# Kernel tuning notes

Hardware: AMD Instinct MI355X
Metric: run time of the kernel (lower is better)

The kernel has to match this reference:

```python
import jax, jax.numpy as jnp
import numpy as np

EPS = 1e-7  # keras backend epsilon


def setup_inputs() -> dict:
    key = jax.random.key(0)
    k1, k2, k3, k4, k5 = jax.random.split(key, 5)
    B, L, D, U = 8, 1024, 256, 256
    seq_data = jax.random.normal(k1, (B, L, D), dtype=jnp.float32)
    graph = jax.random.uniform(k2, (B, L, L), dtype=jnp.float32)
    scale = 1.0 / np.sqrt(D)
    e_weight = jax.random.normal(k3, (D, U), dtype=jnp.float32) * scale
    Wx = jax.random.normal(k4, (U, U), dtype=jnp.float32) * scale
    Wh = jax.random.normal(k5, (U, U), dtype=jnp.float32) * scale
    b = jnp.zeros((U,), dtype=jnp.float32)
    return {"seq_data": seq_data, "graph": graph, "e_weight": e_weight,
            "Wx": Wx, "Wh": Wh, "b": b}


def reference(seq_data, graph, e_weight, Wx, Wh, b):
    # beta = seq_data @ e_weight : (B, L, U)
    beta = jnp.einsum('bld,du->blu', seq_data, e_weight)
    # normalize_graph_output: divide by out-degree sum over axis 2 -> (B, L)
    norm = jnp.maximum(jnp.sum(graph, axis=2), EPS)
    beta = beta / norm[:, :, None]
    # K.batch_dot(beta(B,L,U), graph(B,L,M), axes=(1,1)) -> (B,U,M), then
    # permute (0,2,1) -> (B,M,U); fused as a single einsum.
    agg = jnp.einsum('blu,blm->bmu', beta, graph)  # (B, L, U)
    B, L, U = agg.shape
    h0 = jnp.zeros((B, U), dtype=agg.dtype)  # get_initial_state: zeros

    def step(h, x):  # SimpleRNNCell: h' = tanh(x Wx + h Wh + b)
        h = jnp.tanh(x @ Wx + h @ Wh + b)
        return h, h

    _, ys = jax.lax.scan(step, h0, jnp.swapaxes(agg, 0, 1))  # (L, B, U)
    return jnp.swapaxes(ys, 0, 1)  # (B, L, U)
```

## Files before the change

### kernel.cpp

```cpp
#include <hip/hip_runtime.h>
#include <hip/hip_bf16.h>


typedef unsigned short u16;
typedef unsigned int u32;
typedef __bf16 bf16_t;
typedef __bf16 bf16x8 __attribute__((ext_vector_type(8)));
typedef float f32x4 __attribute__((ext_vector_type(4)));
typedef unsigned short u16x8 __attribute__((ext_vector_type(8)));
typedef unsigned short u16x4 __attribute__((ext_vector_type(4)));

#define LDS_P 72
#define HP_B  288

struct HiLo { u16 hi, lo; };

__device__ __forceinline__ u16 f2bf(float f) {
  bf16_t h = (bf16_t)f;
  return __builtin_bit_cast(u16, h);
}
__device__ __forceinline__ HiLo splitf(float v) {
  bf16_t h = (bf16_t)v;
  HiLo r;
  r.hi = __builtin_bit_cast(u16, h);
  r.lo = f2bf(v - (float)h);
  return r;
}
__device__ __forceinline__ float tanh_fast(float x) {
  float ax = fabsf(x);
  float e  = __expf(-2.0f * ax);
  float t  = __fdividef(1.0f - e, 1.0f + e);
  return copysignf(t, x);
}
__device__ __forceinline__ void sync_lds_only() {
  __asm__ volatile("s_waitcnt lgkmcnt(0)\ns_barrier" ::: "memory");
}

__global__ __launch_bounds__(512, 2) void front1(
    const float* __restrict__ Wx, u16* __restrict__ Wxth, u16* __restrict__ Wxtl,
    const float* __restrict__ Wh, u16* __restrict__ Whth, u16* __restrict__ Whtl,
    const float* __restrict__ graph, float* __restrict__ rnorm,
    const float* __restrict__ seq, const float* __restrict__ E,
    u16* __restrict__ betaTh, u16* __restrict__ betaTl) {
  __shared__ u16 Ah[64 * LDS_P], Al[64 * LDS_P];
  __shared__ u16 Bh[128 * LDS_P], Bl[128 * LDS_P];
  const int bid = blockIdx.x;
  const int t = threadIdx.x;

  if (bid >= 256 && bid < 512) {
    const int wbid = bid - 256;
    const int u = ((wbid & 127) << 1) + (t >> 8), d = t & 255;
    const float* s; u16 *dh, *dl;
    if (wbid < 128) { s = Wx; dh = Wxth; dl = Wxtl; }
    else            { s = Wh; dh = Whth; dl = Whtl; }
    HiLo r = splitf(s[d * 256 + u]);
    dh[u * 256 + d] = r.hi;
    dl[u * 256 + d] = r.lo;
    return;
  }
  if (bid >= 512) {
    const int wave = t >> 6, lane = t & 63;
    const int row = (bid - 512) * 8 + wave;
    const float* p = graph + (size_t)row * 1024 + lane * 16;
    float s = 0.f;
#pragma unroll
    for (int c = 0; c < 4; c++) {
      f32x4 v = *(const f32x4*)(p + c * 4);
#pragma unroll
      for (int j = 0; j < 4; j++) s += v[j];
    }
#pragma unroll
    for (int off = 32; off > 0; off >>= 1) s += __shfl_xor(s, off);
    if (lane == 0) rnorm[row] = 1.0f / fmaxf(s, 1e-7f);
    return;
  }

  const int v = bid;
  const int w = t >> 6, lane = t & 63, quad = lane >> 4, l16 = lane & 15;
  const int msub = w & 3, nsub = w >> 2;
  const int r0 = (v >> 1) * 64, n_base = (v & 1) * 128;
  f32x4 acc[4];
#pragma unroll
  for (int i = 0; i < 4; i++) acc[i] = (f32x4){0.f, 0.f, 0.f, 0.f};

  for (int kb = 0; kb < 256; kb += 64) {
#pragma unroll
    for (int cc = 0; cc < 2; cc++) {
      int c = t + cc * 512;
      int r = c >> 4, c4 = c & 15;
      f32x4 vv = *(const f32x4*)(seq + (size_t)(r0 + r) * 256 + kb + c4 * 4);
      u16x4 hi, lo;
#pragma unroll
      for (int j = 0; j < 4; j++) {
        HiLo s = splitf(vv[j]);
        hi[j] = s.hi; lo[j] = s.lo;
      }
      *(u16x4*)(Ah + r * LDS_P + c4 * 4) = hi;
      *(u16x4*)(Al + r * LDS_P + c4 * 4) = lo;
    }
#pragma unroll
    for (int cc = 0; cc < 4; cc++) {
      int c = t + cc * 512;
      int r = c >> 5, c5 = c & 31;
      f32x4 vv = *(const f32x4*)(E + (size_t)(kb + r) * 256 + n_base + c5 * 4);
#pragma unroll
      for (int j = 0; j < 4; j++) {
        HiLo s = splitf(vv[j]);
        Bh[(c5 * 4 + j) * LDS_P + r] = s.hi;
        Bl[(c5 * 4 + j) * LDS_P + r] = s.lo;
      }
    }
    __syncthreads();
#pragma unroll
    for (int kk = 0; kk < 64; kk += 32) {
      bf16x8 ah = __builtin_bit_cast(bf16x8, *(const u16x8*)(Ah + (msub * 16 + l16) * LDS_P + kk + quad * 8));
      bf16x8 al = __builtin_bit_cast(bf16x8, *(const u16x8*)(Al + (msub * 16 + l16) * LDS_P + kk + quad * 8));
#pragma unroll
      for (int tN = 0; tN < 4; tN++) {
        int brow = nsub * 64 + tN * 16 + l16;
        bf16x8 bh = __builtin_bit_cast(bf16x8, *(const u16x8*)(Bh + brow * LDS_P + kk + quad * 8));
        bf16x8 bl = __builtin_bit_cast(bf16x8, *(const u16x8*)(Bl + brow * LDS_P + kk + quad * 8));
        acc[tN] = __builtin_amdgcn_mfma_f32_16x16x32_bf16(ah, bh, acc[tN], 0, 0, 0);
        acc[tN] = __builtin_amdgcn_mfma_f32_16x16x32_bf16(ah, bl, acc[tN], 0, 0, 0);
        acc[tN] = __builtin_amdgcn_mfma_f32_16x16x32_bf16(al, bh, acc[tN], 0, 0, 0);
      }
    }
    __syncthreads();
  }
  const int rbase = r0 + msub * 16 + quad * 4;
  const int bI = rbase >> 10, lI = rbase & 1023;
#pragma unroll
  for (int tN = 0; tN < 4; tN++) {
    int u = n_base + nsub * 64 + tN * 16 + l16;
    u16x4 hv, lv;
#pragma unroll
    for (int i = 0; i < 4; i++) {
      HiLo s = splitf(acc[tN][i]);
      hv[i] = s.hi; lv[i] = s.lo;
    }
    size_t off = ((size_t)bI << 18) + (size_t)u * 1024 + lI;
    *(u16x4*)(betaTh + off) = hv;
    *(u16x4*)(betaTl + off) = lv;
  }
}

__global__ __launch_bounds__(512, 2) void gemm_agg(const float* __restrict__ graph,
                                                   const u16* __restrict__ betaTh,
                                                   const u16* __restrict__ betaTl,
                                                   const float* __restrict__ rnorm,
                                                   float* __restrict__ agg) {
  __shared__ u16 Ah[64 * LDS_P], Al[64 * LDS_P];
  __shared__ u16 Bh[128 * LDS_P], Bl[128 * LDS_P];
  const int t = threadIdx.x;
  const int w = t >> 6, lane = t & 63, quad = lane >> 4, l16 = lane & 15;
  const int msub = w & 3, nsub = w >> 2;
  const int m0 = blockIdx.x * 64, n_base = blockIdx.y * 128, b = blockIdx.z;
  const float* g = graph + (size_t)b * (1024 * 1024);
  const float* rnb = rnorm + b * 1024;
  const size_t bt = (size_t)b << 18;
  f32x4 acc[4];
#pragma unroll
  for (int i = 0; i < 4; i++) acc[i] = (f32x4){0.f, 0.f, 0.f, 0.f};

  for (int kb = 0; kb < 1024; kb += 64) {
#pragma unroll
    for (int cc = 0; cc < 2; cc++) {
      int c = t + cc * 512;
      int r = c >> 4, c4 = c & 15;
      f32x4 vv = *(const f32x4*)(g + (size_t)(kb + r) * 1024 + m0 + c4 * 4);
      float rn = rnb[kb + r];
#pragma unroll
      for (int j = 0; j < 4; j++) {
        HiLo s = splitf(vv[j] * rn);
        Ah[(c4 * 4 + j) * LDS_P + r] = s.hi;
        Al[(c4 * 4 + j) * LDS_P + r] = s.lo;
      }
    }
#pragma unroll
    for (int cc = 0; cc < 2; cc++) {
      int c = t + cc * 512;
      int r = c >> 3, c8 = c & 7;
      *(u16x8*)(Bh + r * LDS_P + c8 * 8) =
          *(const u16x8*)(betaTh + bt + (size_t)(n_base + r) * 1024 + kb + c8 * 8);
      *(u16x8*)(Bl + r * LDS_P + c8 * 8) =
          *(const u16x8*)(betaTl + bt + (size_t)(n_base + r) * 1024 + kb + c8 * 8);
    }
    __syncthreads();
#pragma unroll
    for (int kk = 0; kk < 64; kk += 32) {
      bf16x8 ah = __builtin_bit_cast(bf16x8, *(const u16x8*)(Ah + (msub * 16 + l16) * LDS_P + kk + quad * 8));
      bf16x8 al = __builtin_bit_cast(bf16x8, *(const u16x8*)(Al + (msub * 16 + l16) * LDS_P + kk + quad * 8));
#pragma unroll
      for (int tN = 0; tN < 4; tN++) {
        int brow = nsub * 64 + tN * 16 + l16;
        bf16x8 bh = __builtin_bit_cast(bf16x8, *(const u16x8*)(Bh + brow * LDS_P + kk + quad * 8));
        bf16x8 bl = __builtin_bit_cast(bf16x8, *(const u16x8*)(Bl + brow * LDS_P + kk + quad * 8));
        acc[tN] = __builtin_amdgcn_mfma_f32_16x16x32_bf16(ah, bh, acc[tN], 0, 0, 0);
        acc[tN] = __builtin_amdgcn_mfma_f32_16x16x32_bf16(ah, bl, acc[tN], 0, 0, 0);
        acc[tN] = __builtin_amdgcn_mfma_f32_16x16x32_bf16(al, bh, acc[tN], 0, 0, 0);
      }
    }
    __syncthreads();
  }
  const int mbase = m0 + msub * 16 + quad * 4;
#pragma unroll
  for (int tN = 0; tN < 4; tN++) {
    int u = n_base + nsub * 64 + tN * 16 + l16;
#pragma unroll
    for (int i = 0; i < 4; i++)
      agg[((size_t)b * 1024 + mbase + i) * 256 + u] = acc[tN][i];
  }
}

__global__ __launch_bounds__(512, 2) void gemm_xpre(const float* __restrict__ agg,
                                                    const u16* __restrict__ Wxth,
                                                    const u16* __restrict__ Wxtl,
                                                    const float* __restrict__ bias,
                                                    float* __restrict__ Xpre) {
  __shared__ u16 Ah[64 * LDS_P], Al[64 * LDS_P];
  __shared__ u16 Bh[128 * LDS_P], Bl[128 * LDS_P];
  const int t = threadIdx.x;
  const int w = t >> 6, lane = t & 63, quad = lane >> 4, l16 = lane & 15;
  const int msub = w & 3, nsub = w >> 2;
  const int r0 = blockIdx.x * 64, n_base = blockIdx.y * 128;
  f32x4 acc[4];
#pragma unroll
  for (int i = 0; i < 4; i++) acc[i] = (f32x4){0.f, 0.f, 0.f, 0.f};

  for (int kb = 0; kb < 256; kb += 64) {
#pragma unroll
    for (int cc = 0; cc < 2; cc++) {
      int c = t + cc * 512;
      int r = c >> 4, c4 = c & 15;
      f32x4 vv = *(const f32x4*)(agg + (size_t)(r0 + r) * 256 + kb + c4 * 4);
      u16x4 hi, lo;
#pragma unroll
      for (int j = 0; j < 4; j++) {
        HiLo s = splitf(vv[j]);
        hi[j] = s.hi; lo[j] = s.lo;
      }
      *(u16x4*)(Ah + r * LDS_P + c4 * 4) = hi;
      *(u16x4*)(Al + r * LDS_P + c4 * 4) = lo;
    }
#pragma unroll
    for (int cc = 0; cc < 2; cc++) {
      int c = t + cc * 512;
      int r = c >> 3, c8 = c & 7;
      *(u16x8*)(Bh + r * LDS_P + c8 * 8) =
          *(const u16x8*)(Wxth + (size_t)(n_base + r) * 256 + kb + c8 * 8);
      *(u16x8*)(Bl + r * LDS_P + c8 * 8) =
          *(const u16x8*)(Wxtl + (size_t)(n_base + r) * 256 + kb + c8 * 8);
    }
    __syncthreads();
#pragma unroll
    for (int kk = 0; kk < 64; kk += 32) {
      bf16x8 ah = __builtin_bit_cast(bf16x8, *(const u16x8*)(Ah + (msub * 16 + l16) * LDS_P + kk + quad * 8));
      bf16x8 al = __builtin_bit_cast(bf16x8, *(const u16x8*)(Al + (msub * 16 + l16) * LDS_P + kk + quad * 8));
#pragma unroll
      for (int tN = 0; tN < 4; tN++) {
        int brow = nsub * 64 + tN * 16 + l16;
        bf16x8 bh = __builtin_bit_cast(bf16x8, *(const u16x8*)(Bh + brow * LDS_P + kk + quad * 8));
        bf16x8 bl = __builtin_bit_cast(bf16x8, *(const u16x8*)(Bl + brow * LDS_P + kk + quad * 8));
        acc[tN] = __builtin_amdgcn_mfma_f32_16x16x32_bf16(ah, bh, acc[tN], 0, 0, 0);
        acc[tN] = __builtin_amdgcn_mfma_f32_16x16x32_bf16(ah, bl, acc[tN], 0, 0, 0);
        acc[tN] = __builtin_amdgcn_mfma_f32_16x16x32_bf16(al, bh, acc[tN], 0, 0, 0);
      }
    }
    __syncthreads();
  }
  const int rbase = r0 + msub * 16 + quad * 4;
  const int bI = rbase >> 10;
#pragma unroll
  for (int tN = 0; tN < 4; tN++) {
    int u = n_base + nsub * 64 + tN * 16 + l16;
    float bu = bias[u];
#pragma unroll
    for (int i = 0; i < 4; i++) {
      int mI = (rbase + i) & 1023;
      Xpre[((size_t)mI * 8 + bI) * 256 + u] = acc[tN][i] + bu;
    }
  }
}

__global__ __launch_bounds__(512, 2) void rnn_scan(const u16* __restrict__ Whth,
                                                   const u16* __restrict__ Whtl,
                                                   const float* __restrict__ Xpre,
                                                   float* __restrict__ out) {
  __shared__ u16 h2[2][2 * HP_B];
  const int b = blockIdx.x;
  const int t = threadIdx.x;
  const int w = t >> 6, lane = t & 63, quad = lane >> 4, l16 = lane & 15;
  const int colbase = w * 32;
  const bool epi = (quad < 2);
  const int col_e = colbase + quad * 16 + l16;

  bf16x8 bwh[2][8], bwl[2][8];
#pragma unroll
  for (int tN = 0; tN < 2; tN++) {
    const u16* wph = Whth + (size_t)(colbase + tN * 16 + l16) * 256 + quad * 8;
    const u16* wpl = Whtl + (size_t)(colbase + tN * 16 + l16) * 256 + quad * 8;
#pragma unroll
    for (int kb = 0; kb < 8; kb++) {
      bwh[tN][kb] = __builtin_bit_cast(bf16x8, *(const u16x8*)(wph + kb * 32));
      bwl[tN][kb] = __builtin_bit_cast(bf16x8, *(const u16x8*)(wpl + kb * 32));
    }
  }
  for (int i = t; i < 2 * 2 * HP_B; i += 512) ((u16*)h2)[i] = 0;

  float cb[4];
  if (epi) {
#pragma unroll
    for (int k = 0; k < 4; k++) cb[k] = Xpre[(size_t)k * 2048 + b * 256 + col_e];
  }
  const float* ldp = Xpre + 4 * 2048 + b * 256 + col_e;
  float* outp = out + (size_t)b * 262144 + col_e;
  const u16* rb0 = &h2[0][(l16 & 1) * HP_B + quad * 8];
  const u16* rb1 = &h2[1][(l16 & 1) * HP_B + quad * 8];
  u16* wb0 = &h2[0][0];
  u16* wb1 = &h2[1][0];
  __syncthreads();

  for (int m4 = 0; m4 < 1024; m4 += 4) {
#pragma unroll
    for (int k = 0; k < 4; k++) {
      const int p = k & 1;
      const u16* rb = p ? rb1 : rb0;
      u16* hw = p ? wb0 : wb1;

      bf16x8 af[8];
#pragma unroll
      for (int kb = 0; kb < 8; kb++)
        af[kb] = __builtin_bit_cast(bf16x8, *(const u16x8*)(rb + kb * 32));

      f32x4 a0a = {0.f,0.f,0.f,0.f}, a0b = {0.f,0.f,0.f,0.f};
      f32x4 a1a = {0.f,0.f,0.f,0.f}, a1b = {0.f,0.f,0.f,0.f};
#pragma unroll
      for (int kb = 0; kb < 4; kb++) {
        a0a = __builtin_amdgcn_mfma_f32_16x16x32_bf16(af[kb], bwh[0][kb], a0a, 0, 0, 0);
        a1a = __builtin_amdgcn_mfma_f32_16x16x32_bf16(af[kb], bwh[1][kb], a1a, 0, 0, 0);
        a0b = __builtin_amdgcn_mfma_f32_16x16x32_bf16(af[kb + 4], bwh[0][kb + 4], a0b, 0, 0, 0);
        a1b = __builtin_amdgcn_mfma_f32_16x16x32_bf16(af[kb + 4], bwh[1][kb + 4], a1b, 0, 0, 0);
        a0a = __builtin_amdgcn_mfma_f32_16x16x32_bf16(af[kb], bwl[0][kb], a0a, 0, 0, 0);
        a1a = __builtin_amdgcn_mfma_f32_16x16x32_bf16(af[kb], bwl[1][kb], a1a, 0, 0, 0);
        a0b = __builtin_amdgcn_mfma_f32_16x16x32_bf16(af[kb + 4], bwl[0][kb + 4], a0b, 0, 0, 0);
        a1b = __builtin_amdgcn_mfma_f32_16x16x32_bf16(af[kb + 4], bwl[1][kb + 4], a1b, 0, 0, 0);
      }

      if (epi) {
        float sA0 = quad ? a1a[0] : a0a[0];
        float sA1 = quad ? a1a[1] : a0a[1];
        float sB0 = quad ? a1b[0] : a0b[0];
        float sB1 = quad ? a1b[1] : a0b[1];
        float hi_part = sA0 + sB0;
        float lo_part = sA1 + sB1;
        float x = (hi_part + lo_part) + cb[k];
        float y = tanh_fast(x);
        HiLo s = splitf(y);
        hw[col_e] = s.hi;
        hw[HP_B + col_e] = s.lo;
        *outp = y;
        if (m4 <= 1019 - k) {
          cb[k] = *ldp;
          ldp += 2048;
        }
      }
      outp += 256;
      sync_lds_only();
    }
  }
}

extern "C" void kernel_launch(void* const* d_in, const int* in_sizes, int n_in,
                              void* d_out, int out_size, void* d_ws, size_t ws_size,
                              hipStream_t stream) {
  (void)in_sizes; (void)n_in; (void)out_size; (void)ws_size;
  const float* seq   = (const float*)d_in[0];
  const float* graph = (const float*)d_in[1];
  const float* E     = (const float*)d_in[2];
  const float* Wx    = (const float*)d_in[3];
  const float* Wh    = (const float*)d_in[4];
  const float* bias  = (const float*)d_in[5];
  float* out = (float*)d_out;

  char* w = (char*)d_ws;
  float* rnorm  = (float*)(w + 0);
  u16*   Wxth   = (u16*)(w + 294912);
  u16*   Wxtl   = (u16*)(w + 425984);
  u16*   Whth   = (u16*)(w + 557056);
  u16*   Whtl   = (u16*)(w + 688128);
  u16*   betaTh = (u16*)(w + 819200);
  u16*   betaTl = (u16*)(w + 5013504);
  float* agg    = (float*)(w + 9207808);
  float* Xpre   = (float*)(w + 17596416);

  front1<<<1536, 512, 0, stream>>>(Wx, Wxth, Wxtl, Wh, Whth, Whtl,
                                   graph, rnorm, seq, E, betaTh, betaTl);
  gemm_agg<<<dim3(16, 2, 8), 512, 0, stream>>>(graph, betaTh, betaTl, rnorm, agg);
  gemm_xpre<<<dim3(128, 2), 512, 0, stream>>>(agg, Wxth, Wxtl, bias, Xpre);
  rnn_scan<<<dim3(8), 512, 0, stream>>>(Whth, Whtl, Xpre, out);
}
```

Measured before the change: 773.5 us.

## Fuse agg, Xpre GEMMs and RNN scan into one kernel with per-tile flags

Merges the aggregation GEMM, the input-projection GEMM and the recurrent scan into a single 136-block launch. 128 producer blocks each compute one 64-row m-tile for one batch across both N halves, write Xpre, then bump an atomic counter for that tile. 8 scan blocks spin on the counters, so the serial scan can begin as soon as the first time tiles are ready instead of waiting for both GEMMs to finish. This removes two launch boundaries and overlaps the GEMM work with the latency-bound scan. In exchange each producer block now does twice the work serially, and the design relies on all 136 blocks being co-resident to avoid deadlock.

```diff
diff --git a/kernel.cpp b/kernel.cpp
--- a/kernel.cpp
+++ b/kernel.cpp
@@ -35,19 +35,28 @@
 __device__ __forceinline__ void sync_lds_only() {
   __asm__ volatile("s_waitcnt lgkmcnt(0)\ns_barrier" ::: "memory");
 }
+__device__ __forceinline__ void wait_tile(volatile unsigned int* xpref, int tl) {
+  while (__hip_atomic_load(&xpref[tl], __ATOMIC_ACQUIRE,
+                           __HIP_MEMORY_SCOPE_AGENT) < 8u) {
+    __builtin_amdgcn_s_sleep(4);
+  }
+  __threadfence();
+}
 
 __global__ __launch_bounds__(512, 2) void front1(
     const float* __restrict__ Wx, u16* __restrict__ Wxth, u16* __restrict__ Wxtl,
     const float* __restrict__ Wh, u16* __restrict__ Whth, u16* __restrict__ Whtl,
     const float* __restrict__ graph, float* __restrict__ rnorm,
     const float* __restrict__ seq, const float* __restrict__ E,
-    u16* __restrict__ betaTh, u16* __restrict__ betaTl) {
+    u16* __restrict__ betaTh, u16* __restrict__ betaTl,
+    unsigned int* __restrict__ xpref) {
   __shared__ u16 Ah[64 * LDS_P], Al[64 * LDS_P];
   __shared__ u16 Bh[128 * LDS_P], Bl[128 * LDS_P];
   const int bid = blockIdx.x;
   const int t = threadIdx.x;
 
   if (bid >= 256 && bid < 512) {
+    if (bid == 256 && t < 16) xpref[t] = 0;
     const int wbid = bid - 256;
     const int u = ((wbid & 127) << 1) + (t >> 8), d = t & 255;
     const float* s; u16 *dh, *dl;
@@ -144,151 +153,159 @@
   }
 }
 
-__global__ __launch_bounds__(512, 2) void gemm_agg(const float* __restrict__ graph,
-                                                   const u16* __restrict__ betaTh,
-                                                   const u16* __restrict__ betaTl,
-                                                   const float* __restrict__ rnorm,
-                                                   float* __restrict__ agg) {
+__global__ __launch_bounds__(512, 2) void back_fused(
+    const float* __restrict__ graph,
+    const u16* __restrict__ betaTh, const u16* __restrict__ betaTl,
+    const float* __restrict__ rnorm, float* __restrict__ agg,
+    const u16* __restrict__ Wxth, const u16* __restrict__ Wxtl,
+    const float* __restrict__ bias, float* __restrict__ Xpre,
+    const u16* __restrict__ Whth, const u16* __restrict__ Whtl,
+    float* __restrict__ out, unsigned int* __restrict__ xpref) {
   __shared__ u16 Ah[64 * LDS_P], Al[64 * LDS_P];
   __shared__ u16 Bh[128 * LDS_P], Bl[128 * LDS_P];
+  __shared__ u16 h2[2][2 * HP_B];
+  const int pid = blockIdx.x;
   const int t = threadIdx.x;
-  const int w = t >> 6, lane = t & 63, quad = lane >> 4, l16 = lane & 15;
-  const int msub = w & 3, nsub = w >> 2;
-  const int m0 = blockIdx.x * 64, n_base = blockIdx.y * 128, b = blockIdx.z;
-  const float* g = graph + (size_t)b * (1024 * 1024);
-  const float* rnb = rnorm + b * 1024;
-  const size_t bt = (size_t)b << 18;
-  f32x4 acc[4];
-#pragma unroll
-  for (int i = 0; i < 4; i++) acc[i] = (f32x4){0.f, 0.f, 0.f, 0.f};
-
-  for (int kb = 0; kb < 1024; kb += 64) {
-#pragma unroll
-    for (int cc = 0; cc < 2; cc++) {
-      int c = t + cc * 512;
-      int r = c >> 4, c4 = c & 15;
-      f32x4 vv = *(const f32x4*)(g + (size_t)(kb + r) * 1024 + m0 + c4 * 4);
-      float rn = rnb[kb + r];
-#pragma unroll
-      for (int j = 0; j < 4; j++) {
-        HiLo s = splitf(vv[j] * rn);
-        Ah[(c4 * 4 + j) * LDS_P + r] = s.hi;
-        Al[(c4 * 4 + j) * LDS_P + r] = s.lo;
-      }
-    }
-#pragma unroll
-    for (int cc = 0; cc < 2; cc++) {
-      int c = t + cc * 512;
-      int r = c >> 3, c8 = c & 7;
-      *(u16x8*)(Bh + r * LDS_P + c8 * 8) =
-          *(const u16x8*)(betaTh + bt + (size_t)(n_base + r) * 1024 + kb + c8 * 8);
-      *(u16x8*)(Bl + r * LDS_P + c8 * 8) =
-          *(const u16x8*)(betaTl + bt + (size_t)(n_base + r) * 1024 + kb + c8 * 8);
-    }
+
+  if (pid < 128) {
+    const int mtile = pid >> 3, b = pid & 7;
+    const int m0 = mtile * 64;
+    const int w = t >> 6, lane = t & 63, quad = lane >> 4, l16 = lane & 15;
+    const int msub = w & 3, nsub = w >> 2;
+    const float* g = graph + (size_t)b * (1024 * 1024);
+    const float* rnb = rnorm + b * 1024;
+    const size_t bt = (size_t)b << 18;
+
+    for (int half = 0; half < 2; ++half) {
+      const int n_base = half * 128;
+      f32x4 acc[4];
+#pragma unroll
+      for (int i = 0; i < 4; i++) acc[i] = (f32x4){0.f, 0.f, 0.f, 0.f};
+
+      for (int kb = 0; kb < 1024; kb += 64) {
+#pragma unroll
+        for (int cc = 0; cc < 2; cc++) {
+          int c = t + cc * 512;
+          int r = c >> 4, c4 = c & 15;
+          f32x4 vv = *(const f32x4*)(g + (size_t)(kb + r) * 1024 + m0 + c4 * 4);
+          float rn = rnb[kb + r];
+#pragma unroll
+          for (int j = 0; j < 4; j++) {
+            HiLo s = splitf(vv[j] * rn);
+            Ah[(c4 * 4 + j) * LDS_P + r] = s.hi;
+            Al[(c4 * 4 + j) * LDS_P + r] = s.lo;
+          }
+        }
+#pragma unroll
+        for (int cc = 0; cc < 2; cc++) {
+          int c = t + cc * 512;
+          int r = c >> 3, c8 = c & 7;
+          *(u16x8*)(Bh + r * LDS_P + c8 * 8) =
+              *(const u16x8*)(betaTh + bt + (size_t)(n_base + r) * 1024 + kb + c8 * 8);
+          *(u16x8*)(Bl + r * LDS_P + c8 * 8) =
+              *(const u16x8*)(betaTl + bt + (size_t)(n_base + r) * 1024 + kb + c8 * 8);
+        }
+        __syncthreads();
+#pragma unroll
+        for (int kk = 0; kk < 64; kk += 32) {
+          bf16x8 ah = __builtin_bit_cast(bf16x8, *(const u16x8*)(Ah + (msub * 16 + l16) * LDS_P + kk + quad * 8));
+          bf16x8 al = __builtin_bit_cast(bf16x8, *(const u16x8*)(Al + (msub * 16 + l16) * LDS_P + kk + quad * 8));
+#pragma unroll
+          for (int tN = 0; tN < 4; tN++) {
+            int brow = nsub * 64 + tN * 16 + l16;
+            bf16x8 bh = __builtin_bit_cast(bf16x8, *(const u16x8*)(Bh + brow * LDS_P + kk + quad * 8));
+            bf16x8 bl = __builtin_bit_cast(bf16x8, *(const u16x8*)(Bl + brow * LDS_P + kk + quad * 8));
+            acc[tN] = __builtin_amdgcn_mfma_f32_16x16x32_bf16(ah, bh, acc[tN], 0, 0, 0);
+            acc[tN] = __builtin_amdgcn_mfma_f32_16x16x32_bf16(ah, bl, acc[tN], 0, 0, 0);
+            acc[tN] = __builtin_amdgcn_mfma_f32_16x16x32_bf16(al, bh, acc[tN], 0, 0, 0);
+          }
+        }
+        __syncthreads();
+      }
+      const int mbase = m0 + msub * 16 + quad * 4;
+#pragma unroll
+      for (int tN = 0; tN < 4; tN++) {
+        int u = n_base + nsub * 64 + tN * 16 + l16;
+#pragma unroll
+        for (int i = 0; i < 4; i++)
+          agg[((size_t)b * 1024 + mbase + i) * 256 + u] = acc[tN][i];
+      }
+    }
+    __asm__ volatile("s_waitcnt vmcnt(0)" ::: "memory");
     __syncthreads();
-#pragma unroll
-    for (int kk = 0; kk < 64; kk += 32) {
-      bf16x8 ah = __builtin_bit_cast(bf16x8, *(const u16x8*)(Ah + (msub * 16 + l16) * LDS_P + kk + quad * 8));
-      bf16x8 al = __builtin_bit_cast(bf16x8, *(const u16x8*)(Al + (msub * 16 + l16) * LDS_P + kk + quad * 8));
+
+    const int r0 = b * 1024 + m0;
+    for (int half = 0; half < 2; ++half) {
+      const int n_base = half * 128;
+      f32x4 acc[4];
+#pragma unroll
+      for (int i = 0; i < 4; i++) acc[i] = (f32x4){0.f, 0.f, 0.f, 0.f};
+
+      for (int kb = 0; kb < 256; kb += 64) {
+#pragma unroll
+        for (int cc = 0; cc < 2; cc++) {
+          int c = t + cc * 512;
+          int r = c >> 4, c4 = c & 15;
+          f32x4 vv = *(const f32x4*)(agg + (size_t)(r0 + r) * 256 + kb + c4 * 4);
+          u16x4 hi, lo;
+#pragma unroll
+          for (int j = 0; j < 4; j++) {
+            HiLo s = splitf(vv[j]);
+            hi[j] = s.hi; lo[j] = s.lo;
+          }
+          *(u16x4*)(Ah + r * LDS_P + c4 * 4) = hi;
+          *(u16x4*)(Al + r * LDS_P + c4 * 4) = lo;
+        }
+#pragma unroll
+        for (int cc = 0; cc < 2; cc++) {
+          int c = t + cc * 512;
+          int r = c >> 3, c8 = c & 7;
+          *(u16x8*)(Bh + r * LDS_P + c8 * 8) =
+              *(const u16x8*)(Wxth + (size_t)(n_base + r) * 256 + kb + c8 * 8);
+          *(u16x8*)(Bl + r * LDS_P + c8 * 8) =
+              *(const u16x8*)(Wxtl + (size_t)(n_base + r) * 256 + kb + c8 * 8);
+        }
+        __syncthreads();
+#pragma unroll
+        for (int kk = 0; kk < 64; kk += 32) {
+          bf16x8 ah = __builtin_bit_cast(bf16x8, *(const u16x8*)(Ah + (msub * 16 + l16) * LDS_P + kk + quad * 8));
+          bf16x8 al = __builtin_bit_cast(bf16x8, *(const u16x8*)(Al + (msub * 16 + l16) * LDS_P + kk + quad * 8));
+#pragma unroll
+          for (int tN = 0; tN < 4; tN++) {
+            int brow = nsub * 64 + tN * 16 + l16;
+            bf16x8 bh = __builtin_bit_cast(bf16x8, *(const u16x8*)(Bh + brow * LDS_P + kk + quad * 8));
+            bf16x8 bl = __builtin_bit_cast(bf16x8, *(const u16x8*)(Bl + brow * LDS_P + kk + quad * 8));
+            acc[tN] = __builtin_amdgcn_mfma_f32_16x16x32_bf16(ah, bh, acc[tN], 0, 0, 0);
+            acc[tN] = __builtin_amdgcn_mfma_f32_16x16x32_bf16(ah, bl, acc[tN], 0, 0, 0);
+            acc[tN] = __builtin_amdgcn_mfma_f32_16x16x32_bf16(al, bh, acc[tN], 0, 0, 0);
+          }
+        }
+        __syncthreads();
+      }
+      const int rbase = r0 + msub * 16 + quad * 4;
+      const int bI = rbase >> 10;
 #pragma unroll
       for (int tN = 0; tN < 4; tN++) {
-        int brow = nsub * 64 + tN * 16 + l16;
-        bf16x8 bh = __builtin_bit_cast(bf16x8, *(const u16x8*)(Bh + brow * LDS_P + kk + quad * 8));
-        bf16x8 bl = __builtin_bit_cast(bf16x8, *(const u16x8*)(Bl + brow * LDS_P + kk + quad * 8));
-        acc[tN] = __builtin_amdgcn_mfma_f32_16x16x32_bf16(ah, bh, acc[tN], 0, 0, 0);
-        acc[tN] = __builtin_amdgcn_mfma_f32_16x16x32_bf16(ah, bl, acc[tN], 0, 0, 0);
-        acc[tN] = __builtin_amdgcn_mfma_f32_16x16x32_bf16(al, bh, acc[tN], 0, 0, 0);
-      }
-    }
+        int u = n_base + nsub * 64 + tN * 16 + l16;
+        float bu = bias[u];
+#pragma unroll
+        for (int i = 0; i < 4; i++) {
+          int mI = (rbase + i) & 1023;
+          Xpre[((size_t)mI * 8 + bI) * 256 + u] = acc[tN][i] + bu;
+        }
+      }
+    }
+    __asm__ volatile("s_waitcnt vmcnt(0)" ::: "memory");
     __syncthreads();
-  }
-  const int mbase = m0 + msub * 16 + quad * 4;
-#pragma unroll
-  for (int tN = 0; tN < 4; tN++) {
-    int u = n_base + nsub * 64 + tN * 16 + l16;
-#pragma unroll
-    for (int i = 0; i < 4; i++)
-      agg[((size_t)b * 1024 + mbase + i) * 256 + u] = acc[tN][i];
-  }
-}
-
-__global__ __launch_bounds__(512, 2) void gemm_xpre(const float* __restrict__ agg,
-                                                    const u16* __restrict__ Wxth,
-                                                    const u16* __restrict__ Wxtl,
-                                                    const float* __restrict__ bias,
-                                                    float* __restrict__ Xpre) {
-  __shared__ u16 Ah[64 * LDS_P], Al[64 * LDS_P];
-  __shared__ u16 Bh[128 * LDS_P], Bl[128 * LDS_P];
-  const int t = threadIdx.x;
-  const int w = t >> 6, lane = t & 63, quad = lane >> 4, l16 = lane & 15;
-  const int msub = w & 3, nsub = w >> 2;
-  const int r0 = blockIdx.x * 64, n_base = blockIdx.y * 128;
-  f32x4 acc[4];
-#pragma unroll
-  for (int i = 0; i < 4; i++) acc[i] = (f32x4){0.f, 0.f, 0.f, 0.f};
-
-  for (int kb = 0; kb < 256; kb += 64) {
-#pragma unroll
-    for (int cc = 0; cc < 2; cc++) {
-      int c = t + cc * 512;
-      int r = c >> 4, c4 = c & 15;
-      f32x4 vv = *(const f32x4*)(agg + (size_t)(r0 + r) * 256 + kb + c4 * 4);
-      u16x4 hi, lo;
-#pragma unroll
-      for (int j = 0; j < 4; j++) {
-        HiLo s = splitf(vv[j]);
-        hi[j] = s.hi; lo[j] = s.lo;
-      }
-      *(u16x4*)(Ah + r * LDS_P + c4 * 4) = hi;
-      *(u16x4*)(Al + r * LDS_P + c4 * 4) = lo;
-    }
-#pragma unroll
-    for (int cc = 0; cc < 2; cc++) {
-      int c = t + cc * 512;
-      int r = c >> 3, c8 = c & 7;
-      *(u16x8*)(Bh + r * LDS_P + c8 * 8) =
-          *(const u16x8*)(Wxth + (size_t)(n_base + r) * 256 + kb + c8 * 8);
-      *(u16x8*)(Bl + r * LDS_P + c8 * 8) =
-          *(const u16x8*)(Wxtl + (size_t)(n_base + r) * 256 + kb + c8 * 8);
-    }
-    __syncthreads();
-#pragma unroll
-    for (int kk = 0; kk < 64; kk += 32) {
-      bf16x8 ah = __builtin_bit_cast(bf16x8, *(const u16x8*)(Ah + (msub * 16 + l16) * LDS_P + kk + quad * 8));
-      bf16x8 al = __builtin_bit_cast(bf16x8, *(const u16x8*)(Al + (msub * 16 + l16) * LDS_P + kk + quad * 8));
-#pragma unroll
-      for (int tN = 0; tN < 4; tN++) {
-        int brow = nsub * 64 + tN * 16 + l16;
-        bf16x8 bh = __builtin_bit_cast(bf16x8, *(const u16x8*)(Bh + brow * LDS_P + kk + quad * 8));
-        bf16x8 bl = __builtin_bit_cast(bf16x8, *(const u16x8*)(Bl + brow * LDS_P + kk + quad * 8));
-        acc[tN] = __builtin_amdgcn_mfma_f32_16x16x32_bf16(ah, bh, acc[tN], 0, 0, 0);
-        acc[tN] = __builtin_amdgcn_mfma_f32_16x16x32_bf16(ah, bl, acc[tN], 0, 0, 0);
-        acc[tN] = __builtin_amdgcn_mfma_f32_16x16x32_bf16(al, bh, acc[tN], 0, 0, 0);
-      }
-    }
-    __syncthreads();
-  }
-  const int rbase = r0 + msub * 16 + quad * 4;
-  const int bI = rbase >> 10;
-#pragma unroll
-  for (int tN = 0; tN < 4; tN++) {
-    int u = n_base + nsub * 64 + tN * 16 + l16;
-    float bu = bias[u];
-#pragma unroll
-    for (int i = 0; i < 4; i++) {
-      int mI = (rbase + i) & 1023;
-      Xpre[((size_t)mI * 8 + bI) * 256 + u] = acc[tN][i] + bu;
-    }
-  }
-}
-
-__global__ __launch_bounds__(512, 2) void rnn_scan(const u16* __restrict__ Whth,
-                                                   const u16* __restrict__ Whtl,
-                                                   const float* __restrict__ Xpre,
-                                                   float* __restrict__ out) {
-  __shared__ u16 h2[2][2 * HP_B];
-  const int b = blockIdx.x;
-  const int t = threadIdx.x;
+    if (t == 0) {
+      __threadfence();
+      __hip_atomic_fetch_add(&xpref[mtile], 1u, __ATOMIC_RELEASE,
+                             __HIP_MEMORY_SCOPE_AGENT);
+    }
+    return;
+  }
+
+  const int b = pid - 128;
   const int w = t >> 6, lane = t & 63, quad = lane >> 4, l16 = lane & 15;
   const int colbase = w * 32;
   const bool epi = (quad < 2);
@@ -309,6 +326,7 @@
 
   float cb[4];
   if (epi) {
+    wait_tile(xpref, 0);
 #pragma unroll
     for (int k = 0; k < 4; k++) cb[k] = Xpre[(size_t)k * 2048 + b * 256 + col_e];
   }
@@ -360,6 +378,8 @@
         hw[HP_B + col_e] = s.lo;
         *outp = y;
         if (m4 <= 1019 - k) {
+          const int nr = m4 + k + 4;
+          if ((nr & 63) == 0) wait_tile(xpref, nr >> 6);
           cb[k] = *ldp;
           ldp += 2048;
         }
@@ -384,6 +404,7 @@
 
   char* w = (char*)d_ws;
   float* rnorm  = (float*)(w + 0);
+  unsigned int* xpref = (unsigned int*)(w + 32768);
   u16*   Wxth   = (u16*)(w + 294912);
   u16*   Wxtl   = (u16*)(w + 425984);
   u16*   Whth   = (u16*)(w + 557056);
@@ -394,8 +415,8 @@
   float* Xpre   = (float*)(w + 17596416);
 
   front1<<<1536, 512, 0, stream>>>(Wx, Wxth, Wxtl, Wh, Whth, Whtl,
-                                   graph, rnorm, seq, E, betaTh, betaTl);
-  gemm_agg<<<dim3(16, 2, 8), 512, 0, stream>>>(graph, betaTh, betaTl, rnorm, agg);
-  gemm_xpre<<<dim3(128, 2), 512, 0, stream>>>(agg, Wxth, Wxtl, bias, Xpre);
-  rnn_scan<<<dim3(8), 512, 0, stream>>>(Whth, Whtl, Xpre, out);
-}
+                                   graph, rnorm, seq, E, betaTh, betaTl, xpref);
+  back_fused<<<136, 512, 0, stream>>>(graph, betaTh, betaTl, rnorm, agg,
+                                      Wxth, Wxtl, bias, Xpre,
+                                      Whth, Whtl, out, xpref);
+}
```

After: 861.7 us. 1.11x slower.
